# Performance work log

Hardware: AMD Instinct MI355X
Metric: run time of the kernel (lower is better)

## Reference

```python
import jax, jax.numpy as jnp
import numpy as np

IN_FEATURES = 1024
OUT_FEATURES = 64
DEGREE = 3
NUM_KNOTS = 10
BATCH = 8192
K0 = NUM_KNOTS + DEGREE  # number of basis columns / control points per edge


def b_spline_basis(x, knots, degree):
    """Vectorized Cox-de Boor recursion.
    x: (..., ) values in [0,1]; knots: (K0+1,).
    Returns (..., K0) basis; last `degree` columns are zero-padded (matches
    control_points width of num_knots+degree as in the original module).
    """
    t = knots
    n0 = t.shape[0] - 1  # = K0 degree-0 intervals
    xe = x[..., None]
    basis = ((xe >= t[:-1]) & (xe < t[1:])).astype(x.dtype)  # (..., K0)
    for p in range(1, degree + 1):
        ti = t[: n0 - p]
        tip = t[p:n0]
        ti1 = t[1 : n0 - p + 1]
        tip1 = t[p + 1 : n0 + 1]
        d1 = jnp.where(tip - ti > 0, tip - ti, jnp.ones_like(ti))
        d2 = jnp.where(tip1 - ti1 > 0, tip1 - ti1, jnp.ones_like(ti1))
        left = jnp.where(tip - ti > 0, (xe - ti) / d1, 0.0) * basis[..., : n0 - p]
        right = jnp.where(tip1 - ti1 > 0, (tip1 - xe) / d2, 0.0) * basis[..., 1 : n0 - p + 1]
        new = left + right
        pad = jnp.zeros(x.shape + (p,), x.dtype)
        basis = jnp.concatenate([new, pad], axis=-1)
    return basis


def setup_inputs() -> dict:
    key = jax.random.key(0)
    k1, k2 = jax.random.split(key)
    x = jax.random.uniform(k1, (BATCH, IN_FEATURES), dtype=jnp.float32)
    knots = jnp.linspace(0.0, 1.0, NUM_KNOTS + DEGREE + 1, dtype=jnp.float32)
    control_points = jax.random.normal(k2, (OUT_FEATURES, IN_FEATURES, K0), dtype=jnp.float32)
    return {"x": x, "knots": knots, "control_points": control_points}


def reference(x, knots, control_points):
    # basis: (B, in, K0) computed once per input feature (original recomputes
    # it out_features times inside a double loop -- same math, fused here).
    basis = b_spline_basis(x, knots, DEGREE)
    # outputs[b, o] = sum_j sum_k basis[b, j, k] * control_points[o, j, k]
    return jnp.einsum("bjk,ojk->bo", basis, control_points)
```

## Files before the change

kernel.cpp:

```cpp
#include <hip/hip_runtime.h>
#include <hip/hip_bf16.h>
#include <stdint.h>

#define IN_F   1024
#define OUT_F  64
#define BATCH  8192
#define BM     128
#define NTHR   256
#define JSPLIT 32
#define JPB    (IN_F / JSPLIT)
#define JC     4
#define NCH    (JPB / JC)
#define BT_BYTES  (JC * 2048)
#define X_BYTES   (BM * JC * 4)
#define BUF_BYTES (BT_BYTES + X_BYTES)
#define OUTSZ  (BATCH * OUT_F)

typedef __attribute__((ext_vector_type(8)))  short short8;
typedef __attribute__((ext_vector_type(16))) float f32x16;

__global__ void kan_prep(const float* __restrict__ cp, __hip_bfloat16* __restrict__ bt) {
    int j = blockIdx.x * 4 + (threadIdx.x >> 6);
    int o = threadIdx.x & 63;
    const float* src = cp + ((size_t)o * IN_F + j) * 13;
    float v[16];
#pragma unroll
    for (int k = 0; k < 10; ++k) v[k] = src[k];
#pragma unroll
    for (int k = 10; k < 16; ++k) v[k] = 0.0f;
    __hip_bfloat16* dst = bt + (size_t)j * 1024;
#pragma unroll
    for (int kh = 0; kh < 2; ++kh)
#pragma unroll
        for (int e = 0; e < 8; ++e)
            dst[kh * 512 + o * 8 + e] = __float2bfloat16(v[kh * 8 + e]);
}

__device__ __forceinline__ uint64_t window64(uint64_t V, int p) {
    uint64_t l = V << ((uint32_t)p & 63);
    uint64_t r = V >> ((uint32_t)(-p) & 63);
    uint64_t f = (p >= 0) ? l : r;
    f = ((uint32_t)(p + 63) <= 126u) ? f : 0ull;
    return f;
}

template<bool PART>
__launch_bounds__(NTHR, 6)
__global__ void kan_main(const float* __restrict__ x,
                         const __hip_bfloat16* __restrict__ bt,
                         void* __restrict__ outp) {
    __shared__ __attribute__((aligned(16))) char lds[2 * BUF_BYTES];

    const int tid   = threadIdx.x;
    const int w     = tid >> 6;
    const int lane  = tid & 63;
    const int l31   = lane & 31;
    const int khalf = lane >> 5;
    const int c0    = 48 + ((khalf << 3) << 4);

    const int r0 = blockIdx.x * BM;
    const int j0 = blockIdx.y * JPB;

    const char*  btg = (const char*)bt + (size_t)j0 * 2048;
    const float* xg  = x + (size_t)(r0 + (tid >> 1)) * IN_F + j0 + (tid & 1) * 2;

    uint4  g0, g1;
    float2 gx;

#define LOAD(ch) do {                                            \
        const char* cb = btg + (ch) * BT_BYTES + tid * 16;       \
        g0 = *(const uint4*)(cb);                                \
        g1 = *(const uint4*)(cb + 4096);                         \
        gx = *(const float2*)(xg + (ch) * JC);                   \
    } while (0)

#define WRITE(boff) do {                                         \
        char* d = lds + (boff) + tid * 16;                       \
        *(uint4*)(d)        = g0;                                \
        *(uint4*)(d + 4096) = g1;                                \
        *(float2*)(lds + (boff) + BT_BYTES + tid * 8) = gx;      \
    } while (0)

    f32x16 acc0, acc1;
#pragma unroll
    for (int i = 0; i < 16; ++i) { acc0[i] = 0.0f; acc1[i] = 0.0f; }

    LOAD(0);
    WRITE(0);
    LOAD(1);
    __syncthreads();

    int cur = 0;
#pragma unroll 1
    for (int ch = 0; ch < NCH; ++ch) {
        if (ch + 1 < NCH) WRITE(cur ^ BUF_BYTES);
        if (ch + 2 < NCH) LOAD(ch + 2);

        {
            const char* base = lds + cur;
            float xv[4];
            *(float4*)&xv[0] = *(const float4*)(base + BT_BYTES + (w * 32 + l31) * 16);
            const char* bbb = base + (khalf << 10) + l31 * 16;
#pragma unroll
            for (int jl = 0; jl < JC; ++jl) {
                const short8 b0 = *(const short8*)(bbb + jl * 2048);
                const short8 b1 = *(const short8*)(bbb + jl * 2048 + 512);

                const float t = xv[jl] * 13.0f;
                float uu;
                asm("v_fract_f32 %0, %1" : "=v"(uu) : "v"(t));
                const int m = (int)t;
                float u2  = uu * uu;
                float omu = 1.0f - uu;
                float o2  = omu * omu;
                float B3  = u2 * (uu * (1.0f / 6.0f));
                float B0  = o2 * (omu * (1.0f / 6.0f));
                float B1  = __builtin_fmaf(u2, __builtin_fmaf(uu, 0.5f, -1.0f), 2.0f / 3.0f);
                float B2  = 1.0f - B0 - B1 - B3;
                uint32_t P01, P23;
                asm("v_cvt_pk_bf16_f32 %0, %1, %2" : "=v"(P01) : "v"(B0), "v"(B1));
                asm("v_cvt_pk_bf16_f32 %0, %1, %2" : "=v"(P23) : "v"(B2), "v"(B3));
                const uint64_t V = ((uint64_t)P23 << 32) | (uint64_t)P01;
                const int p = (m << 4) - c0;
                union { uint64_t q[2]; short8 s; } cv;
                cv.q[0] = window64(V, p);
                cv.q[1] = window64(V, p - 64);

                acc0 = __builtin_amdgcn_mfma_f32_32x32x16_bf16(cv.s, b0, acc0, 0, 0, 0);
                acc1 = __builtin_amdgcn_mfma_f32_32x32x16_bf16(cv.s, b1, acc1, 0, 0, 0);
            }
        }

        if (ch + 1 < NCH) __syncthreads();
        cur ^= BUF_BYTES;
    }
#undef LOAD
#undef WRITE

    if (PART) {
        __hip_bfloat16* op = (__hip_bfloat16*)outp + (size_t)blockIdx.y * OUTSZ;
#pragma unroll
        for (int r = 0; r < 16; ++r) {
            int row = (r & 3) + 8 * (r >> 2) + 4 * khalf;
            __hip_bfloat16* po = op + (size_t)(r0 + w * 32 + row) * OUT_F;
            po[l31]      = __float2bfloat16(acc0[r]);
            po[l31 + 32] = __float2bfloat16(acc1[r]);
        }
    } else {
        float* op = (float*)outp;
#pragma unroll
        for (int r = 0; r < 16; ++r) {
            int row = (r & 3) + 8 * (r >> 2) + 4 * khalf;
            float* po = op + (size_t)(r0 + w * 32 + row) * OUT_F;
            atomicAdd(po + l31,      acc0[r]);
            atomicAdd(po + l31 + 32, acc1[r]);
        }
    }
}

__global__ void kan_reduce(const __hip_bfloat16* __restrict__ part,
                           float* __restrict__ out) {
    const int i = (blockIdx.x * 256 + threadIdx.x) * 8;
    float s[8] = {0, 0, 0, 0, 0, 0, 0, 0};
#pragma unroll
    for (int b = 0; b < JSPLIT; ++b) {
        const short8 v = *(const short8*)(part + (size_t)b * OUTSZ + i);
#pragma unroll
        for (int e = 0; e < 8; ++e) {
            union { uint32_t u; float f; } c;
            c.u = ((uint32_t)(uint16_t)v[e]) << 16;
            s[e] += c.f;
        }
    }
    float4 lo = {s[0], s[1], s[2], s[3]}, hi = {s[4], s[5], s[6], s[7]};
    *(float4*)(out + i)     = lo;
    *(float4*)(out + i + 4) = hi;
}

extern "C" void kernel_launch(void* const* d_in, const int* in_sizes, int n_in,
                              void* d_out, int out_size, void* d_ws, size_t ws_size,
                              hipStream_t stream) {
    const float* x  = (const float*)d_in[0];
    const float* cp = (const float*)d_in[2];
    float* out = (float*)d_out;
    __hip_bfloat16* bt   = (__hip_bfloat16*)d_ws;
    __hip_bfloat16* part = (__hip_bfloat16*)((char*)d_ws + 2u * 1024u * 1024u);

    const size_t need = 2u * 1024u * 1024u + (size_t)JSPLIT * OUTSZ * 2u;
    const bool use_part = ws_size >= need;

    kan_prep<<<dim3(IN_F / 4), dim3(256), 0, stream>>>(cp, bt);
    if (use_part) {
        kan_main<true><<<dim3(BATCH / BM, JSPLIT), dim3(NTHR), 0, stream>>>(x, bt, (void*)part);
        kan_reduce<<<dim3(OUTSZ / 2048), dim3(256), 0, stream>>>(part, out);
    } else {
        hipMemsetAsync(d_out, 0, (size_t)out_size * sizeof(float), stream);
        kan_main<false><<<dim3(BATCH / BM, JSPLIT), dim3(NTHR), 0, stream>>>(x, bt, (void*)d_out);
    }
}
```

Before: 46.51 us.

## Double rows per block so each wave reuses B fragments across two M tiles

Raises the batch tile from 128 to 256 rows. Each wave now computes two 32-row M tiles against the same B fragments (four accumulators), so every LDS read of B feeds four MFMAs instead of two. The x staging switches to one row per thread with a transposed LDS layout, and the window shifting is folded into a helper with simplified masks. This halves the grid and B traffic per output row, at the cost of more accumulator registers and lower occupancy (launch bounds drop from 6 to 4).

```diff
diff --git a/kernel.cpp b/kernel.cpp
--- a/kernel.cpp
+++ b/kernel.cpp
@@ -5,7 +5,7 @@
 #define IN_F   1024
 #define OUT_F  64
 #define BATCH  8192
-#define BM     128
+#define BM     256
 #define NTHR   256
 #define JSPLIT 32
 #define JPB    (IN_F / JSPLIT)
@@ -36,16 +36,36 @@
             dst[kh * 512 + o * 8 + e] = __float2bfloat16(v[kh * 8 + e]);
 }
 
-__device__ __forceinline__ uint64_t window64(uint64_t V, int p) {
-    uint64_t l = V << ((uint32_t)p & 63);
-    uint64_t r = V >> ((uint32_t)(-p) & 63);
-    uint64_t f = (p >= 0) ? l : r;
-    f = ((uint32_t)(p + 63) <= 126u) ? f : 0ull;
-    return f;
+__device__ __forceinline__ short8 afrag(float xv, int c0) {
+    const float t = xv * 13.0f;
+    float uu;
+    asm("v_fract_f32 %0, %1" : "=v"(uu) : "v"(t));
+    const int m = (int)t;
+    const float u2 = uu * uu;
+    const float omu = 1.0f - uu;
+    const float o2 = omu * omu;
+    const float B3 = u2 * (uu * (1.0f / 6.0f));
+    const float B0 = o2 * (omu * (1.0f / 6.0f));
+    const float B1 = __builtin_fmaf(u2, __builtin_fmaf(uu, 0.5f, -1.0f), 2.0f / 3.0f);
+    const float B2 = 1.0f - B0 - B1 - B3;
+    uint32_t P01, P23;
+    asm("v_cvt_pk_bf16_f32 %0, %1, %2" : "=v"(P01) : "v"(B0), "v"(B1));
+    asm("v_cvt_pk_bf16_f32 %0, %1, %2" : "=v"(P23) : "v"(B2), "v"(B3));
+    const uint64_t V = ((uint64_t)P23 << 32) | (uint64_t)P01;
+    const int p = (m << 4) - c0;
+    const uint64_t sl = V << ((uint32_t)p & 63);
+    const uint64_t sr = V >> ((uint32_t)(-p) & 63);
+    const uint64_t t0 = (p < 0) ? sr : sl;
+    const uint64_t q0 = ((uint32_t)(p + 63) < 127u) ? t0 : 0ull;
+    const uint64_t t1 = (p < 64) ? sr : sl;
+    const uint64_t q1 = ((uint32_t)(p - 16) < 112u) ? t1 : 0ull;
+    union { uint64_t q[2]; short8 s; } cv;
+    cv.q[0] = q0; cv.q[1] = q1;
+    return cv.s;
 }
 
 template<bool PART>
-__launch_bounds__(NTHR, 6)
+__launch_bounds__(NTHR, 4)
 __global__ void kan_main(const float* __restrict__ x,
                          const __hip_bfloat16* __restrict__ bt,
                          void* __restrict__ outp) {
@@ -56,34 +76,40 @@
     const int lane  = tid & 63;
     const int l31   = lane & 31;
     const int khalf = lane >> 5;
-    const int c0    = 48 + ((khalf << 3) << 4);
+    const int c0    = 48 + (khalf << 7);
 
     const int r0 = blockIdx.x * BM;
     const int j0 = blockIdx.y * JPB;
 
     const char*  btg = (const char*)bt + (size_t)j0 * 2048;
-    const float* xg  = x + (size_t)(r0 + (tid >> 1)) * IN_F + j0 + (tid & 1) * 2;
+    const float* xg  = x + (size_t)(r0 + tid) * IN_F + j0;
 
     uint4  g0, g1;
-    float2 gx;
+    float4 gx;
 
 #define LOAD(ch) do {                                            \
         const char* cb = btg + (ch) * BT_BYTES + tid * 16;       \
         g0 = *(const uint4*)(cb);                                \
         g1 = *(const uint4*)(cb + 4096);                         \
-        gx = *(const float2*)(xg + (ch) * JC);                   \
+        gx = *(const float4*)(xg + (ch) * JC);                   \
     } while (0)
 
 #define WRITE(boff) do {                                         \
         char* d = lds + (boff) + tid * 16;                       \
         *(uint4*)(d)        = g0;                                \
         *(uint4*)(d + 4096) = g1;                                \
-        *(float2*)(lds + (boff) + BT_BYTES + tid * 8) = gx;      \
+        char* xd = lds + (boff) + BT_BYTES + tid * 4;            \
+        *(float*)(xd)        = gx.x;                             \
+        *(float*)(xd + 1024) = gx.y;                             \
+        *(float*)(xd + 2048) = gx.z;                             \
+        *(float*)(xd + 3072) = gx.w;                             \
     } while (0)
 
-    f32x16 acc0, acc1;
-#pragma unroll
-    for (int i = 0; i < 16; ++i) { acc0[i] = 0.0f; acc1[i] = 0.0f; }
+    f32x16 acc00, acc01, acc10, acc11;
+#pragma unroll
+    for (int i = 0; i < 16; ++i) {
+        acc00[i] = 0.0f; acc01[i] = 0.0f; acc10[i] = 0.0f; acc11[i] = 0.0f;
+    }
 
     LOAD(0);
     WRITE(0);
@@ -98,36 +124,22 @@
 
         {
             const char* base = lds + cur;
-            float xv[4];
-            *(float4*)&xv[0] = *(const float4*)(base + BT_BYTES + (w * 32 + l31) * 16);
+            const char* xb  = base + BT_BYTES + ((w << 6) + l31) * 4;
             const char* bbb = base + (khalf << 10) + l31 * 16;
 #pragma unroll
             for (int jl = 0; jl < JC; ++jl) {
                 const short8 b0 = *(const short8*)(bbb + jl * 2048);
                 const short8 b1 = *(const short8*)(bbb + jl * 2048 + 512);
-
-                const float t = xv[jl] * 13.0f;
-                float uu;
-                asm("v_fract_f32 %0, %1" : "=v"(uu) : "v"(t));
-                const int m = (int)t;
-                float u2  = uu * uu;
-                float omu = 1.0f - uu;
-                float o2  = omu * omu;
-                float B3  = u2 * (uu * (1.0f / 6.0f));
-                float B0  = o2 * (omu * (1.0f / 6.0f));
-                float B1  = __builtin_fmaf(u2, __builtin_fmaf(uu, 0.5f, -1.0f), 2.0f / 3.0f);
-                float B2  = 1.0f - B0 - B1 - B3;
-                uint32_t P01, P23;
-                asm("v_cvt_pk_bf16_f32 %0, %1, %2" : "=v"(P01) : "v"(B0), "v"(B1));
-                asm("v_cvt_pk_bf16_f32 %0, %1, %2" : "=v"(P23) : "v"(B2), "v"(B3));
-                const uint64_t V = ((uint64_t)P23 << 32) | (uint64_t)P01;
-                const int p = (m << 4) - c0;
-                union { uint64_t q[2]; short8 s; } cv;
-                cv.q[0] = window64(V, p);
-                cv.q[1] = window64(V, p - 64);
-
-                acc0 = __builtin_amdgcn_mfma_f32_32x32x16_bf16(cv.s, b0, acc0, 0, 0, 0);
-                acc1 = __builtin_amdgcn_mfma_f32_32x32x16_bf16(cv.s, b1, acc1, 0, 0, 0);
+                const float xv0 = *(const float*)(xb + jl * 1024);
+                const float xv1 = *(const float*)(xb + jl * 1024 + 128);
+
+                const short8 a0 = afrag(xv0, c0);
+                const short8 a1 = afrag(xv1, c0);
+
+                acc00 = __builtin_amdgcn_mfma_f32_32x32x16_bf16(a0, b0, acc00, 0, 0, 0);
+                acc01 = __builtin_amdgcn_mfma_f32_32x32x16_bf16(a0, b1, acc01, 0, 0, 0);
+                acc10 = __builtin_amdgcn_mfma_f32_32x32x16_bf16(a1, b0, acc10, 0, 0, 0);
+                acc11 = __builtin_amdgcn_mfma_f32_32x32x16_bf16(a1, b1, acc11, 0, 0, 0);
             }
         }
 
@@ -141,19 +153,25 @@
         __hip_bfloat16* op = (__hip_bfloat16*)outp + (size_t)blockIdx.y * OUTSZ;
 #pragma unroll
         for (int r = 0; r < 16; ++r) {
-            int row = (r & 3) + 8 * (r >> 2) + 4 * khalf;
-            __hip_bfloat16* po = op + (size_t)(r0 + w * 32 + row) * OUT_F;
-            po[l31]      = __float2bfloat16(acc0[r]);
-            po[l31 + 32] = __float2bfloat16(acc1[r]);
+            const int crow = (r & 3) + 8 * (r >> 2) + 4 * khalf;
+            __hip_bfloat16* p0 = op + (size_t)(r0 + (w << 6) + crow) * OUT_F;
+            __hip_bfloat16* p1 = p0 + 32 * OUT_F;
+            p0[l31]      = __float2bfloat16(acc00[r]);
+            p0[l31 + 32] = __float2bfloat16(acc01[r]);
+            p1[l31]      = __float2bfloat16(acc10[r]);
+            p1[l31 + 32] = __float2bfloat16(acc11[r]);
         }
     } else {
         float* op = (float*)outp;
 #pragma unroll
         for (int r = 0; r < 16; ++r) {
-            int row = (r & 3) + 8 * (r >> 2) + 4 * khalf;
-            float* po = op + (size_t)(r0 + w * 32 + row) * OUT_F;
-            atomicAdd(po + l31,      acc0[r]);
-            atomicAdd(po + l31 + 32, acc1[r]);
+            const int crow = (r & 3) + 8 * (r >> 2) + 4 * khalf;
+            float* p0 = op + (size_t)(r0 + (w << 6) + crow) * OUT_F;
+            float* p1 = p0 + 32 * OUT_F;
+            atomicAdd(p0 + l31,      acc00[r]);
+            atomicAdd(p0 + l31 + 32, acc01[r]);
+            atomicAdd(p1 + l31,      acc10[r]);
+            atomicAdd(p1 + l31 + 32, acc11[r]);
         }
     }
 }
```

Measured after the change: 48.75 us. 4.8% more time.
